# Optimization experiments

Measured on AMD Instinct MI355X. Metric: run time of the kernel, lower is better.

## Reference

```python
import jax, jax.numpy as jnp
import numpy as np


def setup_inputs() -> dict:
    key = jax.random.key(0)
    ks = jax.random.split(key, 5)
    b, t, e, h = 8, 1024, 256, 8
    w = lambda k, shape: jax.random.normal(k, shape, dtype=jnp.float32) * 0.02
    return {
        "x": jax.random.normal(ks[0], (b, t, e), dtype=jnp.float32),
        "Wq": w(ks[1], (e, e * h)), "bq": jnp.zeros((e * h,), jnp.float32),
        "Wk": w(ks[2], (e, e * h)), "bk": jnp.zeros((e * h,), jnp.float32),
        "Wv": w(ks[3], (e, e * h)), "bv": jnp.zeros((e * h,), jnp.float32),
        "Wu": w(ks[4], (e * h, e)), "bu": jnp.zeros((e,), jnp.float32),
    }


def reference(x, Wq, bq, Wk, bk, Wv, bv, Wu, bu):
    b, t, e = x.shape
    h = Wq.shape[1] // e  # each head has FULL width e in this module
    q = (x @ Wq + bq).reshape(b, t, h, e)
    k = (x @ Wk + bk).reshape(b, t, h, e)
    v = (x @ Wv + bv).reshape(b, t, h, e)
    # scores: (b, h, t, t), scaled by sqrt(e) as in the original
    scores = jnp.einsum('bihe,bjhe->bhij', q, k) / jnp.sqrt(jnp.asarray(e, jnp.float32))
    i = jnp.arange(t)[:, None]
    j = jnp.arange(t)[None, :]
    # mask mode 'first': triu(offset=0) -> -inf, i.e. query i sees only j < i
    scores = jnp.where(j >= i, -jnp.inf, scores)
    # row 0 is fully masked (torch softmax -> NaN, then zeroed post-softmax);
    # make it finite first so softmax is well-defined, then zero the attention row
    scores = jnp.where(i == 0, 0.0, scores)
    att = jax.nn.softmax(scores, axis=-1)
    att = jnp.where(i == 0, 0.0, att)
    out = jnp.einsum('bhij,bjhe->bihe', att, v).reshape(b, t, h * e)
    return out @ Wu + bu
```

## Files before the change

kernel.cpp:

```cpp
#include <hip/hip_runtime.h>
#include <hip/hip_bf16.h>

typedef unsigned short u16;
typedef short bf16x8 __attribute__((ext_vector_type(8)));
typedef float f32x4 __attribute__((ext_vector_type(4)));

#define EXP2(x) __builtin_amdgcn_exp2f(x)

static __device__ __forceinline__ u16 f2bf(float f) {
  union { float f; unsigned u; } a; a.f = f;
  unsigned r = a.u + 0x7fffu + ((a.u >> 16) & 1u);
  return (u16)(r >> 16);
}

static __device__ __forceinline__ unsigned pkbf(float a, float b) {
  union { __hip_bfloat162 h; unsigned u; } c;
  c.h = __float22bfloat162_rn(make_float2(a, b));
  return c.u;
}

static __device__ __forceinline__ bf16x8 as_bf(int4 v) {
  union { int4 i; bf16x8 b; } u; u.i = v; return u.b;
}

#define GLDS16(g, l)                                         \
  __builtin_amdgcn_global_load_lds(                          \
      (const __attribute__((address_space(1))) void*)(g),    \
      (__attribute__((address_space(3))) void*)(l), 16, 0, 0)

__global__ __launch_bounds__(256) void prep(
    const float* __restrict__ x, u16* __restrict__ Xb,
    const float* __restrict__ Wq, u16* __restrict__ Wqt,
    const float* __restrict__ Wk, u16* __restrict__ Wkt,
    const float* __restrict__ Wv, u16* __restrict__ Wvt,
    const float* __restrict__ Wu, u16* __restrict__ Wut) {
  const int bid = blockIdx.x, tid = threadIdx.x;
  if (bid < 1024) {
    int i = bid * 256 + tid;
    const float4* p = (const float4*)x + (size_t)i * 2;
    float4 a = p[0], b = p[1];
    union { unsigned s[4]; int4 v; } u2;
    u2.s[0] = pkbf(a.x, a.y); u2.s[1] = pkbf(a.z, a.w);
    u2.s[2] = pkbf(b.x, b.y); u2.s[3] = pkbf(b.z, b.w);
    ((int4*)Xb)[i] = u2.v;
    return;
  }
  const int which = (bid - 1024) >> 6;
  const float* in; u16* out; int R, C;
  if (which == 0)      { in = Wq; out = Wqt; R = 256;  C = 2048; }
  else if (which == 1) { in = Wk; out = Wkt; R = 256;  C = 2048; }
  else if (which == 2) { in = Wv; out = Wvt; R = 256;  C = 2048; }
  else                 { in = Wu; out = Wut; R = 2048; C = 256;  }
  int T = ((bid - 1024) & 63) * 256 + tid;
  int c = T % C;
  int r0 = (T / C) * 32;
  __align__(16) u16 tmp[32];
#pragma unroll
  for (int j = 0; j < 32; ++j) tmp[j] = f2bf(in[(size_t)(r0 + j) * C + c]);
#pragma unroll
  for (int q = 0; q < 4; ++q)
    *(int4*)(out + (size_t)c * R + r0 + q * 8) = *(int4*)&tmp[q * 8];
}

__global__ __launch_bounds__(256) void gemm_qkv(const u16* __restrict__ A,
                                                const u16* __restrict__ Wt,
                                                const float* __restrict__ bq,
                                                const float* __restrict__ bk,
                                                const float* __restrict__ bv,
                                                u16* __restrict__ Qw,
                                                u16* __restrict__ Kw,
                                                u16* __restrict__ Vt) {
  constexpr int BM = 128, BN = 128, BK = 64;
  __shared__ int4 smem4[2048];
  int4* As4 = smem4;
  int4* Bs4 = smem4 + 1024;
  const int tid = threadIdx.x;
  const int w = tid >> 6, lane = tid & 63, lq = lane & 15, quad = lane >> 4;
  const int wm = w >> 1, wn = w & 1;
  const int m0 = blockIdx.y * BM, n0 = blockIdx.x * BN;
  const int z = blockIdx.z;

  const u16* Btz = Wt + (size_t)z * 2048 * 256;
  const float* bias = (z == 0) ? bq : (z == 1 ? bk : bv);

  const int srow = lane >> 3;
  const int scb = (lane & 7) ^ ((lane >> 3) & 7);

  f32x4 acc[4][4];
#pragma unroll
  for (int mi = 0; mi < 4; ++mi)
#pragma unroll
    for (int ni = 0; ni < 4; ++ni) {
      f32x4 z4 = {0.f, 0.f, 0.f, 0.f};
      acc[mi][ni] = z4;
    }

  for (int k0 = 0; k0 < 256; k0 += BK) {
    __syncthreads();
#pragma unroll
    for (int it = 0; it < 4; ++it) {
      int r = (w * 4 + it) * 8 + srow;
      GLDS16(A + (size_t)(m0 + r) * 256 + k0 + scb * 8,
             (char*)As4 + (w * 4 + it) * 1024);
    }
#pragma unroll
    for (int it = 0; it < 4; ++it) {
      int r = (w * 4 + it) * 8 + srow;
      GLDS16(Btz + (size_t)(n0 + r) * 256 + k0 + scb * 8,
             (char*)Bs4 + (w * 4 + it) * 1024);
    }
    __syncthreads();
#pragma unroll
    for (int kk = 0; kk < 2; ++kk) {
      int4 af[4], bf[4];
#pragma unroll
      for (int mi = 0; mi < 4; ++mi) {
        int r = wm * 64 + mi * 16 + lq;
        af[mi] = As4[r * 8 + ((kk * 4 + quad) ^ (lq & 7))];
      }
#pragma unroll
      for (int ni = 0; ni < 4; ++ni) {
        int r = wn * 64 + ni * 16 + lq;
        bf[ni] = Bs4[r * 8 + ((kk * 4 + quad) ^ (lq & 7))];
      }
#pragma unroll
      for (int mi = 0; mi < 4; ++mi)
#pragma unroll
        for (int ni = 0; ni < 4; ++ni)
          acc[mi][ni] = __builtin_amdgcn_mfma_f32_16x16x32_bf16(
              as_bf(af[mi]), as_bf(bf[ni]), acc[mi][ni], 0, 0, 0);
    }
  }

  if (z < 2) {
    u16* Cout = z ? Kw : Qw;
#pragma unroll
    for (int mi = 0; mi < 4; ++mi)
#pragma unroll
      for (int ni = 0; ni < 4; ++ni)
#pragma unroll
        for (int r = 0; r < 4; ++r) {
          int row = m0 + wm * 64 + mi * 16 + quad * 4 + r;
          int col = n0 + wn * 64 + ni * 16 + lq;
          Cout[(size_t)row * 2048 + col] = f2bf(acc[mi][ni][r] + bias[col]);
        }
  } else {
    __syncthreads();
    u16* Ts = (u16*)smem4;
#pragma unroll
    for (int mi = 0; mi < 4; ++mi)
#pragma unroll
      for (int ni = 0; ni < 4; ++ni) {
        int c = wn * 64 + ni * 16 + lq;
        int r0 = wm * 64 + mi * 16 + quad * 4;
        float vb = bias[n0 + c];
        uint2 dd;
        dd.x = pkbf(acc[mi][ni][0] + vb, acc[mi][ni][1] + vb);
        dd.y = pkbf(acc[mi][ni][2] + vb, acc[mi][ni][3] + vb);
        *(uint2*)&Ts[c * 128 + (((r0 >> 3) ^ (c & 15)) << 3) + (r0 & 7)] = dd;
      }
    __syncthreads();
    const int b = m0 >> 10, t0 = m0 & 1023;
    const int e0 = n0 & 255, h = n0 >> 8;
    const int bh = b * 8 + h;
    const int i4 = tid & 15;
#pragma unroll
    for (int cc = 0; cc < 8; ++cc) {
      int c = (tid >> 4) + cc * 16;
      int4 val = *(const int4*)&Ts[c * 128 + ((i4 ^ (c & 15)) << 3)];
      *(int4*)(Vt + (size_t)(bh * 256 + e0 + c) * 1024 + t0 + i4 * 8) = val;
    }
  }
}

template <int BM, int BN>
__global__ __launch_bounds__(256) void gemm_bt(const u16* __restrict__ A,
                                               const u16* __restrict__ Bt,
                                               const float* __restrict__ bias,
                                               float* __restrict__ Cout,
                                               int M, int N, int K) {
  constexpr int BK = 64;
  constexpr int TM = BM / 2 / 16, TN = BN / 2 / 16;
  constexpr int nA = BM / 32, nB = BN / 32;
  __shared__ int4 As4[BM * 8];
  __shared__ int4 Bs4[BN * 8];
  const int tid = threadIdx.x;
  const int w = tid >> 6, lane = tid & 63, lq = lane & 15, quad = lane >> 4;
  const int wm = w >> 1, wn = w & 1;
  const int m0 = blockIdx.y * BM, n0 = blockIdx.x * BN;

  const int srow = lane >> 3;
  const int scb = (lane & 7) ^ ((lane >> 3) & 7);

  f32x4 acc[TM][TN];
#pragma unroll
  for (int mi = 0; mi < TM; ++mi)
#pragma unroll
    for (int ni = 0; ni < TN; ++ni) {
      f32x4 z4 = {0.f, 0.f, 0.f, 0.f};
      acc[mi][ni] = z4;
    }

  for (int k0 = 0; k0 < K; k0 += BK) {
    __syncthreads();
#pragma unroll
    for (int it = 0; it < nA; ++it) {
      int r = (w * nA + it) * 8 + srow;
      GLDS16(A + (size_t)(m0 + r) * K + k0 + scb * 8,
             (char*)As4 + (w * nA + it) * 1024);
    }
#pragma unroll
    for (int it = 0; it < nB; ++it) {
      int r = (w * nB + it) * 8 + srow;
      GLDS16(Bt + (size_t)(n0 + r) * K + k0 + scb * 8,
             (char*)Bs4 + (w * nB + it) * 1024);
    }
    __syncthreads();
#pragma unroll
    for (int kk = 0; kk < BK / 32; ++kk) {
      int4 af[TM], bf[TN];
#pragma unroll
      for (int mi = 0; mi < TM; ++mi) {
        int r = wm * (BM / 2) + mi * 16 + lq;
        af[mi] = As4[r * 8 + ((kk * 4 + quad) ^ (lq & 7))];
      }
#pragma unroll
      for (int ni = 0; ni < TN; ++ni) {
        int r = wn * (BN / 2) + ni * 16 + lq;
        bf[ni] = Bs4[r * 8 + ((kk * 4 + quad) ^ (lq & 7))];
      }
#pragma unroll
      for (int mi = 0; mi < TM; ++mi)
#pragma unroll
        for (int ni = 0; ni < TN; ++ni)
          acc[mi][ni] = __builtin_amdgcn_mfma_f32_16x16x32_bf16(
              as_bf(af[mi]), as_bf(bf[ni]), acc[mi][ni], 0, 0, 0);
    }
  }

#pragma unroll
  for (int mi = 0; mi < TM; ++mi)
#pragma unroll
    for (int ni = 0; ni < TN; ++ni)
#pragma unroll
      for (int r = 0; r < 4; ++r) {
        int row = m0 + wm * (BM / 2) + mi * 16 + quad * 4 + r;
        int col = n0 + wn * (BN / 2) + ni * 16 + lq;
        Cout[(size_t)row * N + col] = acc[mi][ni][r] + bias[col];
      }
}

__global__ __launch_bounds__(256, 2) void attn_kernel(const u16* __restrict__ Q,
                                                      const u16* __restrict__ Km,
                                                      const u16* __restrict__ Vt,
                                                      u16* __restrict__ O) {
  const int bh = blockIdx.x;
  const int pair = blockIdx.y;
  const int b = bh >> 3, h = bh & 7;
  const int tid = threadIdx.x;
  const int w = tid >> 6, lane = tid & 63, lq = lane & 15, quad = lane >> 4;

  __shared__ int4 Ks4[2048];
  __shared__ int4 Vs4[2048];
  __shared__ u16 Ps[4096];
  u16* myPs = Ps + w * 1024;

  int koffb[8], voffb[8];
  {
    const int kg = (lane & 31) >> 3;
#pragma unroll
    for (int it = 0; it < 8; ++it) {
      int r = w * 16 + it * 2 + (lane >> 5);
      int p = (lane & 7) ^ (r & 7);
      koffb[it] = r * 2048 + (kg * 8 + p) * 8;
      int rv = w * 64 + it * 8 + (lane >> 3);
      int cb = (lane & 7) ^ (rv & 7);
      voffb[it] = rv * 1024 + cb * 8;
    }
  }
  const u16* kbase = Km + (size_t)b * 2097152 + h * 256;
  const u16* vbase = Vt + (size_t)bh * 262144;

  const float SCL = 0.09016844f;
  const float NEG = -3.0e38f;

#pragma unroll 1
  for (int hv = 0; hv < 2; ++hv) {
    const int qt = hv ? (15 - pair) : pair;
    const int qg = qt * 64 + w * 16 + lq;
    const u16* qptr = Q + (size_t)(b * 1024 + qg) * 2048 + h * 256 + quad * 8;
    int4 qf[8];
#pragma unroll
    for (int kk = 0; kk < 8; ++kk) qf[kk] = *(const int4*)(qptr + kk * 32);

    f32x4 of[16];
#pragma unroll
    for (int i = 0; i < 16; ++i) {
      f32x4 z = {0.f, 0.f, 0.f, 0.f};
      of[i] = z;
    }
    float mst = NEG, lst = 0.f;

    for (int kt = 0; kt <= qt; ++kt) {
      __syncthreads();
      {
        const u16* kb = kbase + (size_t)kt * 131072;
        const u16* vb = vbase + kt * 64;
#pragma unroll
        for (int it = 0; it < 8; ++it)
          GLDS16(kb + koffb[it], (char*)Ks4 + (w * 8 + it) * 1024);
#pragma unroll
        for (int it = 0; it < 8; ++it)
          GLDS16(vb + voffb[it], (char*)Vs4 + (w * 8 + it) * 1024);
      }
      __syncthreads();

      f32x4 sc[4];
#pragma unroll
      for (int ns = 0; ns < 4; ++ns) {
        f32x4 a = {0.f, 0.f, 0.f, 0.f};
        int r = ns * 16 + lq;
#pragma unroll
        for (int kk = 0; kk < 8; ++kk) {
          int G = kk * 4 + quad;
          int4 kf = Ks4[r * 32 + (G >> 3) * 8 + ((G & 7) ^ (lq & 7))];
          a = __builtin_amdgcn_mfma_f32_16x16x32_bf16(as_bf(kf), as_bf(qf[kk]),
                                                      a, 0, 0, 0);
        }
        sc[ns] = a;
      }
#pragma unroll
      for (int ns = 0; ns < 4; ++ns) {
        int keyb = kt * 64 + ns * 16 + quad * 4;
#pragma unroll
        for (int r = 0; r < 4; ++r) {
          float v = sc[ns][r] * SCL;
          sc[ns][r] = (keyb + r >= qg) ? NEG : v;
        }
      }
      float m16 = sc[0][0];
#pragma unroll
      for (int ns = 0; ns < 4; ++ns)
#pragma unroll
        for (int r = 0; r < 4; ++r) m16 = fmaxf(m16, sc[ns][r]);
      m16 = fmaxf(m16, __shfl_xor(m16, 16));
      m16 = fmaxf(m16, __shfl_xor(m16, 32));
      if (__any(m16 > mst)) {
        float mn = fmaxf(mst, m16);
        float alpha = EXP2(mst - mn);
        mst = mn;
        lst *= alpha;
#pragma unroll
        for (int i = 0; i < 16; ++i)
#pragma unroll
          for (int r = 0; r < 4; ++r) of[i][r] *= alpha;
      }
      float s = 0.f;
#pragma unroll
      for (int ns = 0; ns < 4; ++ns)
#pragma unroll
        for (int r = 0; r < 4; ++r) {
          float p = EXP2(sc[ns][r] - mst);
          sc[ns][r] = p;
          s += p;
        }
      s += __shfl_xor(s, 16);
      s += __shfl_xor(s, 32);
      lst += s;

#pragma unroll
      for (int ns = 0; ns < 4; ++ns) {
        int kb2 = ns * 2 + (quad >> 1);
        int base = lq * 64 + ((kb2 ^ (lq & 7)) << 3) + (quad & 1) * 4;
        *(unsigned*)&myPs[base] = pkbf(sc[ns][0], sc[ns][1]);
        *(unsigned*)&myPs[base + 2] = pkbf(sc[ns][2], sc[ns][3]);
      }
      int4 pf[2];
#pragma unroll
      for (int kk2 = 0; kk2 < 2; ++kk2) {
        int kbp = (kk2 * 4 + quad) ^ (lq & 7);
        pf[kk2] = *(const int4*)&myPs[lq * 64 + kbp * 8];
      }
#pragma unroll
      for (int ns2 = 0; ns2 < 16; ++ns2) {
        int r = ns2 * 16 + lq;
#pragma unroll
        for (int kk2 = 0; kk2 < 2; ++kk2) {
          int4 vf = Vs4[r * 8 + ((kk2 * 4 + quad) ^ (lq & 7))];
          of[ns2] = __builtin_amdgcn_mfma_f32_16x16x32_bf16(
              as_bf(vf), as_bf(pf[kk2]), of[ns2], 0, 0, 0);
        }
      }
    }

    float inv = lst > 0.f ? 1.f / lst : 0.f;
    if (qg == 0) inv = 0.f;
    u16* optr = O + (size_t)(b * 1024 + qg) * 2048 + h * 256 + quad * 4;
#pragma unroll
    for (int ns2 = 0; ns2 < 16; ++ns2) {
      uint2 o4;
      o4.x = pkbf(of[ns2][0] * inv, of[ns2][1] * inv);
      o4.y = pkbf(of[ns2][2] * inv, of[ns2][3] * inv);
      *(uint2*)(optr + ns2 * 16) = o4;
    }
  }
}

#define WS_XB 0
#define WS_WQT 4194304
#define WS_WUT 7340032
#define WS_QW 8388608
#define WS_KW 41943040
#define WS_OW 75497472
#define WS_VTW 109051904

extern "C" void kernel_launch(void* const* d_in, const int* in_sizes, int n_in,
                              void* d_out, int out_size, void* d_ws, size_t ws_size,
                              hipStream_t stream) {
  const float* x = (const float*)d_in[0];
  const float* Wq = (const float*)d_in[1];
  const float* bq = (const float*)d_in[2];
  const float* Wk = (const float*)d_in[3];
  const float* bk = (const float*)d_in[4];
  const float* Wv = (const float*)d_in[5];
  const float* bv = (const float*)d_in[6];
  const float* Wu = (const float*)d_in[7];
  const float* bu = (const float*)d_in[8];
  float* out = (float*)d_out;

  char* ws = (char*)d_ws;
  u16* Xb = (u16*)(ws + WS_XB);
  u16* Wqt = (u16*)(ws + WS_WQT);
  u16* Wkt = Wqt + 524288;
  u16* Wvt = Wqt + 1048576;
  u16* Wut = (u16*)(ws + WS_WUT);
  u16* Qw = (u16*)(ws + WS_QW);
  u16* Kw = (u16*)(ws + WS_KW);
  u16* Ow = (u16*)(ws + WS_OW);
  u16* Vtw = (u16*)(ws + WS_VTW);

  prep<<<1280, 256, 0, stream>>>(x, Xb, Wq, Wqt, Wk, Wkt, Wv, Wvt, Wu, Wut);

  gemm_qkv<<<dim3(16, 64, 3), 256, 0, stream>>>(Xb, Wqt, bq, bk, bv, Qw, Kw, Vtw);

  attn_kernel<<<dim3(64, 8), 256, 0, stream>>>(Qw, Kw, Vtw, Ow);

  gemm_bt<128, 64><<<dim3(4, 64), 256, 0, stream>>>(Ow, Wut, bu, out, 8192, 256, 2048);
}
```

Before: 221.6 us.

## Process 128-query tiles per block with two row groups per wave

Each attention block now handles one 128-query tile, with each wave computing two 16-row query groups, instead of two 64-query tiles processed sequentially. Each loaded K/V tile and each K/V fragment read from LDS is reused by two MFMA streams, which cuts global and LDS traffic per query. Blocks are ordered longest-first for causal load balance. The cost is roughly doubled accumulator registers, which risks spills or lower occupancy, and fewer blocks overall.

```diff
diff --git a/kernel.cpp b/kernel.cpp
--- a/kernel.cpp
+++ b/kernel.cpp
@@ -255,152 +255,180 @@
                                                       const u16* __restrict__ Vt,
                                                       u16* __restrict__ O) {
   const int bh = blockIdx.x;
-  const int pair = blockIdx.y;
+  const int y = blockIdx.y;
+  const int qt = (y < 4) ? (7 - y) : (y - 4);
   const int b = bh >> 3, h = bh & 7;
   const int tid = threadIdx.x;
   const int w = tid >> 6, lane = tid & 63, lq = lane & 15, quad = lane >> 4;
 
   __shared__ int4 Ks4[2048];
   __shared__ int4 Vs4[2048];
-  __shared__ u16 Ps[4096];
-  u16* myPs = Ps + w * 1024;
-
-  int koffb[8], voffb[8];
-  {
-    const int kg = (lane & 31) >> 3;
-#pragma unroll
-    for (int it = 0; it < 8; ++it) {
-      int r = w * 16 + it * 2 + (lane >> 5);
-      int p = (lane & 7) ^ (r & 7);
-      koffb[it] = r * 2048 + (kg * 8 + p) * 8;
-      int rv = w * 64 + it * 8 + (lane >> 3);
-      int cb = (lane & 7) ^ (rv & 7);
-      voffb[it] = rv * 1024 + cb * 8;
-    }
-  }
+  __shared__ u16 Ps[8192];
+  u16* myPs = Ps + w * 2048;
+
   const u16* kbase = Km + (size_t)b * 2097152 + h * 256;
   const u16* vbase = Vt + (size_t)bh * 262144;
 
   const float SCL = 0.09016844f;
   const float NEG = -3.0e38f;
 
-#pragma unroll 1
-  for (int hv = 0; hv < 2; ++hv) {
-    const int qt = hv ? (15 - pair) : pair;
-    const int qg = qt * 64 + w * 16 + lq;
-    const u16* qptr = Q + (size_t)(b * 1024 + qg) * 2048 + h * 256 + quad * 8;
-    int4 qf[8];
-#pragma unroll
-    for (int kk = 0; kk < 8; ++kk) qf[kk] = *(const int4*)(qptr + kk * 32);
-
-    f32x4 of[16];
+  const int q0 = qt * 128 + w * 32;
+  const int qg[2] = {q0 + lq, q0 + 16 + lq};
+
+  int4 qf[2][8];
+#pragma unroll
+  for (int g = 0; g < 2; ++g) {
+    const u16* qptr =
+        Q + (size_t)(b * 1024 + q0 + g * 16 + lq) * 2048 + h * 256 + quad * 8;
+#pragma unroll
+    for (int kk = 0; kk < 8; ++kk) qf[g][kk] = *(const int4*)(qptr + kk * 32);
+  }
+
+  f32x4 of[2][16];
+#pragma unroll
+  for (int g = 0; g < 2; ++g)
 #pragma unroll
     for (int i = 0; i < 16; ++i) {
       f32x4 z = {0.f, 0.f, 0.f, 0.f};
-      of[i] = z;
-    }
-    float mst = NEG, lst = 0.f;
-
-    for (int kt = 0; kt <= qt; ++kt) {
-      __syncthreads();
-      {
-        const u16* kb = kbase + (size_t)kt * 131072;
-        const u16* vb = vbase + kt * 64;
-#pragma unroll
-        for (int it = 0; it < 8; ++it)
-          GLDS16(kb + koffb[it], (char*)Ks4 + (w * 8 + it) * 1024);
-#pragma unroll
-        for (int it = 0; it < 8; ++it)
-          GLDS16(vb + voffb[it], (char*)Vs4 + (w * 8 + it) * 1024);
-      }
-      __syncthreads();
-
-      f32x4 sc[4];
-#pragma unroll
-      for (int ns = 0; ns < 4; ++ns) {
-        f32x4 a = {0.f, 0.f, 0.f, 0.f};
-        int r = ns * 16 + lq;
-#pragma unroll
-        for (int kk = 0; kk < 8; ++kk) {
-          int G = kk * 4 + quad;
-          int4 kf = Ks4[r * 32 + (G >> 3) * 8 + ((G & 7) ^ (lq & 7))];
-          a = __builtin_amdgcn_mfma_f32_16x16x32_bf16(as_bf(kf), as_bf(qf[kk]),
-                                                      a, 0, 0, 0);
-        }
-        sc[ns] = a;
-      }
+      of[g][i] = z;
+    }
+  float mst[2] = {NEG, NEG}, lst[2] = {0.f, 0.f};
+
+  const int niter = 2 * qt + 2;
+#pragma unroll 1
+  for (int kt = 0; kt < niter; ++kt) {
+    __syncthreads();
+    {
+      const u16* kb = kbase + (size_t)kt * 131072;
+      const u16* vb = vbase + kt * 64;
+      const int kg = (lane & 31) >> 3;
+#pragma unroll
+      for (int it = 0; it < 8; ++it) {
+        int r = w * 16 + it * 2 + (lane >> 5);
+        int p = (lane & 7) ^ (r & 7);
+        GLDS16(kb + r * 2048 + (kg * 8 + p) * 8, (char*)Ks4 + (w * 8 + it) * 1024);
+      }
+#pragma unroll
+      for (int it = 0; it < 8; ++it) {
+        int rv = w * 64 + it * 8 + (lane >> 3);
+        int cb = (lane & 7) ^ (rv & 7);
+        GLDS16(vb + rv * 1024 + cb * 8, (char*)Vs4 + (w * 8 + it) * 1024);
+      }
+    }
+    __syncthreads();
+
+    f32x4 sc[2][4];
+#pragma unroll
+    for (int ns = 0; ns < 4; ++ns) {
+      f32x4 a0 = {0.f, 0.f, 0.f, 0.f}, a1 = {0.f, 0.f, 0.f, 0.f};
+      int r = ns * 16 + lq;
+#pragma unroll
+      for (int kk = 0; kk < 8; ++kk) {
+        int G = kk * 4 + quad;
+        int4 kf = Ks4[r * 32 + (G >> 3) * 8 + ((G & 7) ^ (lq & 7))];
+        a0 = __builtin_amdgcn_mfma_f32_16x16x32_bf16(as_bf(kf), as_bf(qf[0][kk]),
+                                                     a0, 0, 0, 0);
+        a1 = __builtin_amdgcn_mfma_f32_16x16x32_bf16(as_bf(kf), as_bf(qf[1][kk]),
+                                                     a1, 0, 0, 0);
+      }
+      sc[0][ns] = a0;
+      sc[1][ns] = a1;
+    }
+#pragma unroll
+    for (int g = 0; g < 2; ++g)
 #pragma unroll
       for (int ns = 0; ns < 4; ++ns) {
         int keyb = kt * 64 + ns * 16 + quad * 4;
 #pragma unroll
         for (int r = 0; r < 4; ++r) {
-          float v = sc[ns][r] * SCL;
-          sc[ns][r] = (keyb + r >= qg) ? NEG : v;
+          float v = sc[g][ns][r] * SCL;
+          sc[g][ns][r] = (keyb + r >= qg[g]) ? NEG : v;
         }
       }
-      float m16 = sc[0][0];
+    float m16[2];
+#pragma unroll
+    for (int g = 0; g < 2; ++g) {
+      float m = sc[g][0][0];
 #pragma unroll
       for (int ns = 0; ns < 4; ++ns)
 #pragma unroll
-        for (int r = 0; r < 4; ++r) m16 = fmaxf(m16, sc[ns][r]);
-      m16 = fmaxf(m16, __shfl_xor(m16, 16));
-      m16 = fmaxf(m16, __shfl_xor(m16, 32));
-      if (__any(m16 > mst)) {
-        float mn = fmaxf(mst, m16);
-        float alpha = EXP2(mst - mn);
-        mst = mn;
-        lst *= alpha;
+        for (int r = 0; r < 4; ++r) m = fmaxf(m, sc[g][ns][r]);
+      m = fmaxf(m, __shfl_xor(m, 16));
+      m = fmaxf(m, __shfl_xor(m, 32));
+      m16[g] = m;
+    }
+    if (__any(m16[0] > mst[0] || m16[1] > mst[1])) {
+#pragma unroll
+      for (int g = 0; g < 2; ++g) {
+        float mn = fmaxf(mst[g], m16[g]);
+        float alpha = EXP2(mst[g] - mn);
+        mst[g] = mn;
+        lst[g] *= alpha;
 #pragma unroll
         for (int i = 0; i < 16; ++i)
 #pragma unroll
-          for (int r = 0; r < 4; ++r) of[i][r] *= alpha;
-      }
+          for (int r = 0; r < 4; ++r) of[g][i][r] *= alpha;
+      }
+    }
+#pragma unroll
+    for (int g = 0; g < 2; ++g) {
       float s = 0.f;
 #pragma unroll
       for (int ns = 0; ns < 4; ++ns)
 #pragma unroll
         for (int r = 0; r < 4; ++r) {
-          float p = EXP2(sc[ns][r] - mst);
-          sc[ns][r] = p;
+          float p = EXP2(sc[g][ns][r] - mst[g]);
+          sc[g][ns][r] = p;
           s += p;
         }
       s += __shfl_xor(s, 16);
       s += __shfl_xor(s, 32);
-      lst += s;
-
+      lst[g] += s;
+    }
+
+#pragma unroll
+    for (int g = 0; g < 2; ++g)
 #pragma unroll
       for (int ns = 0; ns < 4; ++ns) {
         int kb2 = ns * 2 + (quad >> 1);
-        int base = lq * 64 + ((kb2 ^ (lq & 7)) << 3) + (quad & 1) * 4;
-        *(unsigned*)&myPs[base] = pkbf(sc[ns][0], sc[ns][1]);
-        *(unsigned*)&myPs[base + 2] = pkbf(sc[ns][2], sc[ns][3]);
-      }
-      int4 pf[2];
+        int base = g * 1024 + lq * 64 + ((kb2 ^ (lq & 7)) << 3) + (quad & 1) * 4;
+        uint2 dd;
+        dd.x = pkbf(sc[g][ns][0], sc[g][ns][1]);
+        dd.y = pkbf(sc[g][ns][2], sc[g][ns][3]);
+        *(uint2*)&myPs[base] = dd;
+      }
+    int4 pf[2][2];
+#pragma unroll
+    for (int g = 0; g < 2; ++g)
 #pragma unroll
       for (int kk2 = 0; kk2 < 2; ++kk2) {
         int kbp = (kk2 * 4 + quad) ^ (lq & 7);
-        pf[kk2] = *(const int4*)&myPs[lq * 64 + kbp * 8];
-      }
-#pragma unroll
-      for (int ns2 = 0; ns2 < 16; ++ns2) {
-        int r = ns2 * 16 + lq;
-#pragma unroll
-        for (int kk2 = 0; kk2 < 2; ++kk2) {
-          int4 vf = Vs4[r * 8 + ((kk2 * 4 + quad) ^ (lq & 7))];
-          of[ns2] = __builtin_amdgcn_mfma_f32_16x16x32_bf16(
-              as_bf(vf), as_bf(pf[kk2]), of[ns2], 0, 0, 0);
-        }
-      }
-    }
-
-    float inv = lst > 0.f ? 1.f / lst : 0.f;
-    if (qg == 0) inv = 0.f;
-    u16* optr = O + (size_t)(b * 1024 + qg) * 2048 + h * 256 + quad * 4;
+        pf[g][kk2] = *(const int4*)&myPs[g * 1024 + lq * 64 + kbp * 8];
+      }
+#pragma unroll
+    for (int ns2 = 0; ns2 < 16; ++ns2) {
+      int r = ns2 * 16 + lq;
+#pragma unroll
+      for (int kk2 = 0; kk2 < 2; ++kk2) {
+        int4 vf = Vs4[r * 8 + ((kk2 * 4 + quad) ^ (lq & 7))];
+        of[0][ns2] = __builtin_amdgcn_mfma_f32_16x16x32_bf16(
+            as_bf(vf), as_bf(pf[0][kk2]), of[0][ns2], 0, 0, 0);
+        of[1][ns2] = __builtin_amdgcn_mfma_f32_16x16x32_bf16(
+            as_bf(vf), as_bf(pf[1][kk2]), of[1][ns2], 0, 0, 0);
+      }
+    }
+  }
+
+#pragma unroll
+  for (int g = 0; g < 2; ++g) {
+    float inv = lst[g] > 0.f ? 1.f / lst[g] : 0.f;
+    if (qg[g] == 0) inv = 0.f;
+    u16* optr = O + (size_t)(b * 1024 + qg[g]) * 2048 + h * 256 + quad * 4;
 #pragma unroll
     for (int ns2 = 0; ns2 < 16; ++ns2) {
       uint2 o4;
-      o4.x = pkbf(of[ns2][0] * inv, of[ns2][1] * inv);
-      o4.y = pkbf(of[ns2][2] * inv, of[ns2][3] * inv);
+      o4.x = pkbf(of[g][ns2][0] * inv, of[g][ns2][1] * inv);
+      o4.y = pkbf(of[g][ns2][2] * inv, of[g][ns2][3] * inv);
       *(uint2*)(optr + ns2 * 16) = o4;
     }
   }
```

New measurement: 267.4 us. 1.21x slower.
